# Kernel optimization log

Hardware: AMD Instinct MI355X
Metric: run time of the kernel (lower is better)

The kernel has to match this reference:

```python
import jax, jax.numpy as jnp
import numpy as np

S = 64        # state_dim
M = 16        # message_dim
H = 128       # hidden_unit_message_dim
HR = 128      # hidden_unit_readout_dim
NSTEPS = 10
N_NODES = 10000
N_FACTORS = 40000


def setup_inputs() -> dict:
    rng = np.random.default_rng(0)
    n, F = N_NODES, N_FACTORS
    # random undirected factor pairs (u, v) with u < v
    u = rng.integers(0, n - 1, F)
    v = rng.integers(u + 1, n)
    # var->factor directed edges: (u, i) and (v, i) for factor i
    v2f_src = np.stack([u, v], 1).ravel().astype(np.int32)          # [E]
    v2f_dst = np.repeat(np.arange(F), 2).astype(np.int32)           # [E]
    b = rng.normal(size=n).astype(np.float32)
    Juv = rng.normal(size=F).astype(np.float32)
    Jvu = rng.normal(size=F).astype(np.float32)
    feat_u = np.stack([b[u], b[v], Juv, Jvu], 1)
    feat_v = np.stack([b[v], b[u], Juv, Jvu], 1)
    feat = np.stack([feat_u, feat_v], 1).reshape(-1, 4).astype(np.float32)  # [E,4]
    p = lambda *s: (0.1 * rng.normal(size=s)).astype(np.float32)
    z = lambda *s: np.zeros(s, np.float32)
    inp = {
        'v2f_src': jnp.asarray(v2f_src), 'v2f_dst': jnp.asarray(v2f_dst),
        'f2v_src': jnp.asarray(v2f_dst), 'f2v_dst': jnp.asarray(v2f_src),
        'feat_v2f': jnp.asarray(feat), 'feat_f2v': jnp.asarray(feat),
        'n_nodes': n, 'n_factors': F,
        'Qw': jnp.asarray(p(4, M * M)), 'Qb': jnp.asarray(z(M * M)),
        'mp1_w1': jnp.asarray(p(2 * S, H)), 'mp1_b1': jnp.asarray(z(H)),
        'mp1_w2': jnp.asarray(p(H, H)), 'mp1_b2': jnp.asarray(z(H)),
        'mp1_w3': jnp.asarray(p(H, M)), 'mp1_b3': jnp.asarray(z(M)),
        'mp2_w1': jnp.asarray(p(2 * S, H)), 'mp2_b1': jnp.asarray(z(H)),
        'mp2_w2': jnp.asarray(p(H, H)), 'mp2_b2': jnp.asarray(z(H)),
        'mp2_w3': jnp.asarray(p(H, M)), 'mp2_b3': jnp.asarray(z(M)),
        'g1_wih': jnp.asarray(p(M, 3 * S)), 'g1_whh': jnp.asarray(p(S, 3 * S)),
        'g1_bih': jnp.asarray(z(3 * S)), 'g1_bhh': jnp.asarray(z(3 * S)),
        'g2_wih': jnp.asarray(p(M, 3 * S)), 'g2_whh': jnp.asarray(p(S, 3 * S)),
        'g2_bih': jnp.asarray(z(3 * S)), 'g2_bhh': jnp.asarray(z(3 * S)),
        'ro_w1': jnp.asarray(p(S, HR)), 'ro_b1': jnp.asarray(z(HR)),
        'ro_w2': jnp.asarray(p(HR, HR)), 'ro_b2': jnp.asarray(z(HR)),
        'ro_w3': jnp.asarray(p(HR, 2)), 'ro_b3': jnp.asarray(z(2)),
    }
    return inp


def _mlp(x, w1, b1, w2, b2, w3, b3):
    h = jax.nn.relu(x @ w1 + b1)
    h = jax.nn.relu(h @ w2 + b2)
    return h @ w3 + b3


def _gru(x, h, wih, whh, bih, bhh):
    # torch.nn.GRUCell gate order: r, z, n
    gi = x @ wih + bih
    gh = h @ whh + bhh
    ir, iz, inn = jnp.split(gi, 3, axis=-1)
    hr, hz, hn = jnp.split(gh, 3, axis=-1)
    r = jax.nn.sigmoid(ir + hr)
    zg = jax.nn.sigmoid(iz + hz)
    ng = jnp.tanh(inn + r * hn)
    return (1.0 - zg) * ng + zg * h


def reference(v2f_src, v2f_dst, f2v_src, f2v_dst, feat_v2f, feat_f2v,
              n_nodes, n_factors, Qw, Qb,
              mp1_w1, mp1_b1, mp1_w2, mp1_b2, mp1_w3, mp1_b3,
              mp2_w1, mp2_b1, mp2_w2, mp2_b2, mp2_w3, mp2_b3,
              g1_wih, g1_whh, g1_bih, g1_bhh,
              g2_wih, g2_whh, g2_bih, g2_bhh,
              ro_w1, ro_b1, ro_w2, ro_b2, ro_w3, ro_b3):
    var_h = jnp.zeros((n_nodes, S), feat_v2f.dtype)
    fac_h = jnp.zeros((n_factors, S), feat_v2f.dtype)
    # per-edge transform matrices are the same every step; hoist out of the loop
    q1 = (feat_v2f @ Qw + Qb).reshape(-1, M, M)  # [E, M, M]
    q2 = (feat_f2v @ Qw + Qb).reshape(-1, M, M)
    for _ in range(NSTEPS):
        # var -> factor
        x = jnp.concatenate([var_h[v2f_src], fac_h[v2f_dst]], axis=-1)  # [E, 2S]
        m = _mlp(x, mp1_w1, mp1_b1, mp1_w2, mp1_b2, mp1_w3, mp1_b3)    # [E, M]
        m = jnp.einsum('eij,ej->ei', q1, m)
        fac_msg = jax.ops.segment_sum(m, v2f_dst, num_segments=n_factors)
        fac_h = _gru(fac_msg, fac_h, g1_wih, g1_whh, g1_bih, g1_bhh)
        # factor -> var
        x = jnp.concatenate([fac_h[f2v_src], var_h[f2v_dst]], axis=-1)
        m = _mlp(x, mp2_w1, mp2_b1, mp2_w2, mp2_b2, mp2_w3, mp2_b3)
        m = jnp.einsum('eij,ej->ei', q2, m)
        var_msg = jax.ops.segment_sum(m, f2v_dst, num_segments=n_nodes)
        var_h = _gru(var_msg, var_h, g2_wih, g2_whh, g2_bih, g2_bhh)
    out = _mlp(var_h, ro_w1, ro_b1, ro_w2, ro_b2, ro_w3, ro_b3)  # [n_nodes, 2]
    return jax.nn.softmax(out, axis=1)
```

## Files before the change

kernel.cpp:

```cpp
#include <hip/hip_runtime.h>

#define NSTEPS 10

typedef __attribute__((ext_vector_type(8))) short bf16x8;
typedef __attribute__((ext_vector_type(4))) short bf16x4;
typedef __attribute__((ext_vector_type(4))) float f32x4;

__device__ __forceinline__ float sigmoidf_(float x) { return 1.0f / (1.0f + __expf(-x)); }
__device__ __forceinline__ float tanh_fast(float x) {
  const float e = __expf(2.f * x);
  return 1.f - 2.f / (e + 1.f);
}

__device__ __forceinline__ short bf16_(float x) {
  union { float f; unsigned u; } c; c.f = x;
  unsigned r = (c.u + 0x7FFFu + ((c.u >> 16) & 1u)) >> 16;
  return (short)r;
}
__device__ __forceinline__ unsigned pk2_(float a, float b) {
  union { float f; unsigned u; } ca, cb; ca.f = a; cb.f = b;
  return __builtin_amdgcn_perm(cb.u + 0x8000u, ca.u + 0x8000u, 0x07060302u);
}
__device__ __forceinline__ short pk1_(float a) {
  union { float f; unsigned u; } c; c.f = a;
  return (short)((c.u + 0x8000u) >> 16);
}
__device__ __forceinline__ float lo_(unsigned u) { union { unsigned u; float f; } c; c.u = u << 16; return c.f; }
__device__ __forceinline__ float hi_(unsigned u) { union { unsigned u; float f; } c; c.u = u & 0xffff0000u; return c.f; }

__device__ __forceinline__ f32x4 mfma_16x16x32(bf16x8 a, bf16x8 b, f32x4 c) {
  return __builtin_amdgcn_mfma_f32_16x16x32_bf16(a, b, c, 0, 0, 0);
}

struct PackJob { const float* src; int N; int KS; int nchunks; };
struct PackArgs {
  PackJob jb[10];
  const float* Qw; const float* Qb;
  const float* g1wih; const float* g1whh;
  const float* g2wih; const float* g2whh;
};

__global__ __launch_bounds__(256) void k_pack(PackArgs a, short* __restrict__ out, int total) {
  const int g = blockIdx.x * 256 + threadIdx.x;
  if (g >= total) return;
  int c = g >> 9;
  const int r = g & 511;
  const int j = r & 7, n = (r >> 3) & 15, q = (r >> 7) & 3;
  const int kq = q * 8 + j;
  float val = 0.f;
  bool done = false;
  #pragma unroll
  for (int ji = 0; ji < 10; ++ji) {
    if (!done && c < a.jb[ji].nchunks) {
      const int ks = c % a.jb[ji].KS;
      const int nt = c / a.jb[ji].KS;
      const int k = ks * 32 + kq;
      val = a.jb[ji].src[(size_t)k * a.jb[ji].N + nt * 16 + n];
      done = true;
    }
    if (!done) c -= a.jb[ji].nchunks;
  }
  if (!done) {
    if (c < 5) {
      val = 0.f;
      if (kq < 16) val = (c < 4) ? a.Qw[c * 256 + n * 16 + kq] : a.Qb[n * 16 + kq];
    } else {
      c -= 5;
      const float* wih = (c < 48) ? a.g1wih : a.g2wih;
      const float* whh = (c < 48) ? a.g1whh : a.g2whh;
      if (c >= 48) c -= 48;
      const int nt = c / 3, ks = c % 3;
      const int k = ks * 32 + kq;
      const int ng = nt * 16 + n;
      const int gate = ng >> 6, s = ng & 63;
      val = 0.f;
      if (gate == 0) {
        if (k < 16) val = wih[k * 192 + s];
        else if (k < 80) val = whh[(k - 16) * 192 + s];
      } else if (gate == 1) {
        if (k < 16) val = wih[k * 192 + 64 + s];
        else if (k < 80) val = whh[(k - 16) * 192 + 64 + s];
      } else if (gate == 2) {
        if (k < 16) val = wih[k * 192 + 128 + s];
      } else {
        if (k >= 16 && k < 80) val = whh[(k - 16) * 192 + 128 + s];
      }
    }
  }
  out[g] = bf16_(val);
}

__global__ __launch_bounds__(256) void k_dense2(
    const float* __restrict__ X0, const short* __restrict__ W0, short* __restrict__ C0,
    int rows0, int g0,
    const float* __restrict__ X1, const short* __restrict__ W1, short* __restrict__ C1,
    int rows1, float* __restrict__ zeroPtr,
    const float* __restrict__ gruMsg, float* __restrict__ gruH,
    const short* __restrict__ gruW,
    const float* __restrict__ gbih, const float* __restrict__ gbhh)
{
  constexpr int KS = 2, K = 64, STR = K + 8;
  __shared__ short Xs[64 * STR];
  __shared__ short SA[64 * 104];
  const int t = threadIdx.x, lane = t & 63, wave = t >> 6;
  const int m = lane & 15, quad = lane >> 4;

  const float* X; const short* Wf; short* C; int rows, rbase;
  const bool job0 = (int)blockIdx.x < g0;
  if (job0) {
    X = X0; Wf = W0; C = C0; rows = rows0; rbase = blockIdx.x * 64;
  } else {
    X = X1; Wf = W1; C = C1; rows = rows1; rbase = ((int)blockIdx.x - g0) * 64;
    if (zeroPtr) {
      const int zr = rbase + (t >> 2);
      if (zr < rows1) {
        f32x4 z = {0.f, 0.f, 0.f, 0.f};
        *(f32x4*)(zeroPtr + (size_t)zr * 16 + (t & 3) * 4) = z;
      }
    }
  }

  bf16x8 b[2][KS];
  #pragma unroll
  for (int nt2 = 0; nt2 < 2; ++nt2)
    #pragma unroll
    for (int ks = 0; ks < KS; ++ks)
      b[nt2][ks] = ((const bf16x8*)Wf)[((wave * 2 + nt2) * KS + ks) * 64 + lane];

  if (job0 && gruMsg) {
    {
      const int r = t >> 2, q4 = t & 3, rg = rbase + r;
      #pragma unroll
      for (int i = 0; i < 6; ++i) {
        const int c = q4 * 4 + i * 16;
        f32x4 v = {0.f, 0.f, 0.f, 0.f};
        if (rg < rows) {
          if (c < 16)      v = *(const f32x4*)(gruMsg + (size_t)rg * 16 + c);
          else if (c < 80) v = *(const f32x4*)(gruH + (size_t)rg * 64 + (c - 16));
        }
        *(unsigned*)&SA[r * 104 + c]     = pk2_(v.x, v.y);
        *(unsigned*)&SA[r * 104 + c + 2] = pk2_(v.z, v.w);
      }
    }
    __syncthreads();
    f32x4 acc[16] = {};
    #pragma unroll
    for (int ks = 0; ks < 3; ++ks) {
      const bf16x8 a = *(const bf16x8*)&SA[(wave * 16 + m) * 104 + ks * 32 + quad * 8];
      #pragma unroll
      for (int nt = 0; nt < 16; ++nt)
        acc[nt] = mfma_16x16x32(a, ((const bf16x8*)gruW)[(nt * 3 + ks) * 64 + lane], acc[nt]);
    }
    #pragma unroll
    for (int nt = 0; nt < 4; ++nt) {
      const int s = nt * 16 + m;
      const float br  = gbih[s] + gbhh[s];
      const float bz  = gbih[64 + s] + gbhh[64 + s];
      const float bin = gbih[128 + s];
      const float bhn = gbhh[128 + s];
      #pragma unroll
      for (int reg = 0; reg < 4; ++reg) {
        const int lr = wave * 16 + quad * 4 + reg;
        const int rg = rbase + lr;
        short hv = 0;
        if (rg < rows) {
          const float ho = gruH[(size_t)rg * 64 + s];
          const float rr = sigmoidf_(acc[nt][reg] + br);
          const float zz = sigmoidf_(acc[4 + nt][reg] + bz);
          const float nn = tanh_fast(acc[8 + nt][reg] + bin + rr * (acc[12 + nt][reg] + bhn));
          const float hn = (1.f - zz) * nn + zz * ho;
          gruH[(size_t)rg * 64 + s] = hn;
          hv = pk1_(hn);
        }
        Xs[lr * STR + s] = hv;
      }
    }
    __syncthreads();
  } else {
    const int r = t >> 2, q4 = t & 3, rg = rbase + r;
    #pragma unroll
    for (int i = 0; i < K / 16; ++i) {
      const int cc = q4 * 4 + i * 16;
      f32x4 v = {0.f, 0.f, 0.f, 0.f};
      if (rg < rows) v = *(const f32x4*)(X + (size_t)rg * K + cc);
      *(unsigned*)&Xs[r * STR + cc]     = pk2_(v.x, v.y);
      *(unsigned*)&Xs[r * STR + cc + 2] = pk2_(v.z, v.w);
    }
    __syncthreads();
  }

  f32x4 acc[2][4] = {};
  #pragma unroll
  for (int ks = 0; ks < KS; ++ks) {
    bf16x8 afr[4];
    #pragma unroll
    for (int mt = 0; mt < 4; ++mt)
      afr[mt] = *(const bf16x8*)&Xs[(mt * 16 + m) * STR + ks * 32 + quad * 8];
    #pragma unroll
    for (int nt2 = 0; nt2 < 2; ++nt2)
      #pragma unroll
      for (int mt = 0; mt < 4; ++mt)
        acc[nt2][mt] = mfma_16x16x32(afr[mt], b[nt2][ks], acc[nt2][mt]);
  }

  #pragma unroll
  for (int nt2 = 0; nt2 < 2; ++nt2) {
    const int col = (wave * 2 + nt2) * 16 + m;
    #pragma unroll
    for (int mt = 0; mt < 4; ++mt)
      #pragma unroll
      for (int rr = 0; rr < 4; ++rr) {
        const int rg = rbase + mt * 16 + quad * 4 + rr;
        if (rg < rows) C[(size_t)rg * 128 + col] = pk1_(acc[nt2][mt][rr]);
      }
  }
}

template<bool PAIRED>
__global__ __launch_bounds__(256) void k_edge(
    const short* __restrict__ Pa, const short* __restrict__ Pb,
    const int* __restrict__ src, const int* __restrict__ dst,
    const float* __restrict__ feat,
    const float* __restrict__ b1, const float* __restrict__ b2,
    const float* __restrict__ b3,
    const short* __restrict__ w2f, const short* __restrict__ w3f,
    const short* __restrict__ qf,
    float* __restrict__ outMsg,
    float* __restrict__ facH, const short* __restrict__ gruW,
    const float* __restrict__ gbih, const float* __restrict__ gbhh,
    int E, int F)
{
  __shared__ short h1s[64 * 136];
  __shared__ short ms[64 * 40];
  __shared__ short AsG[32 * 104];
  __shared__ float feats[64 * 4];
  __shared__ int sidx[64], didx[64];

  const int t = threadIdx.x, lane = t & 63, wave = t >> 6;
  const int e0 = blockIdx.x * 64;
  const int f0 = e0 >> 1;

  if (t < 64) {
    const int eg = e0 + t;
    sidx[t] = (eg < E) ? src[eg] : 0;
    didx[t] = (eg < E) ? dst[eg] : 0;
  }
  {
    const int e = t >> 2, k = t & 3;
    const int eg = e0 + e;
    feats[e * 4 + k] = (eg < E) ? feat[(size_t)eg * 4 + k] : 0.f;
  }
  if (PAIRED) {
    const int hr = t >> 3, hc = (t & 7) * 8;
    const int f = f0 + hr;
    f32x4 a0 = {0.f,0.f,0.f,0.f}, a1 = {0.f,0.f,0.f,0.f};
    if (f < F) {
      a0 = *(const f32x4*)(facH + (size_t)f * 64 + hc);
      a1 = *(const f32x4*)(facH + (size_t)f * 64 + hc + 4);
    }
    uint4 o;
    o.x = pk2_(a0.x, a0.y); o.y = pk2_(a0.z, a0.w);
    o.z = pk2_(a1.x, a1.y); o.w = pk2_(a1.z, a1.w);
    *(uint4*)&AsG[hr * 104 + 16 + hc] = o;
    if (t < 64) {
      uint4 z = make_uint4(0u, 0u, 0u, 0u);
      *(uint4*)&AsG[(t >> 1) * 104 + 80 + (t & 1) * 8] = z;
    }
  }
  bf16x8 bw2[2][4];
  #pragma unroll
  for (int nt2 = 0; nt2 < 2; ++nt2)
    #pragma unroll
    for (int ks = 0; ks < 4; ++ks)
      bw2[nt2][ks] = ((const bf16x8*)w2f)[((wave * 2 + nt2) * 4 + ks) * 64 + lane];
  __syncthreads();

  {
    const int r = t >> 2, q4 = t & 3;
    const bool ok = (e0 + r) < E;
    const short* pa = Pa + (size_t)sidx[r] * 128;
    const short* pb = Pb + (size_t)didx[r] * 128;
    #pragma unroll
    for (int i = 0; i < 4; ++i) {
      const int col = (q4 + i * 4) * 8;
      uint4 o = make_uint4(0u, 0u, 0u, 0u);
      if (ok) {
        const uint4 ua = *(const uint4*)(pa + col);
        const uint4 ub = *(const uint4*)(pb + col);
        const f32x4 ba = *(const f32x4*)(b1 + col);
        const f32x4 bb = *(const f32x4*)(b1 + col + 4);
        o.x = pk2_(fmaxf(lo_(ua.x) + lo_(ub.x) + ba.x, 0.f),
                   fmaxf(hi_(ua.x) + hi_(ub.x) + ba.y, 0.f));
        o.y = pk2_(fmaxf(lo_(ua.y) + lo_(ub.y) + ba.z, 0.f),
                   fmaxf(hi_(ua.y) + hi_(ub.y) + ba.w, 0.f));
        o.z = pk2_(fmaxf(lo_(ua.z) + lo_(ub.z) + bb.x, 0.f),
                   fmaxf(hi_(ua.z) + hi_(ub.z) + bb.y, 0.f));
        o.w = pk2_(fmaxf(lo_(ua.w) + lo_(ub.w) + bb.z, 0.f),
                   fmaxf(hi_(ua.w) + hi_(ub.w) + bb.w, 0.f));
      }
      *(uint4*)&h1s[r * 136 + col] = o;
    }
  }
  __syncthreads();

  const int m = lane & 15, quad = lane >> 4;

  f32x4 acc2[2][4] = {};
  #pragma unroll
  for (int ks = 0; ks < 4; ++ks) {
    bf16x8 afr[4];
    #pragma unroll
    for (int mt = 0; mt < 4; ++mt)
      afr[mt] = *(const bf16x8*)&h1s[(mt * 16 + m) * 136 + ks * 32 + quad * 8];
    #pragma unroll
    for (int nt2 = 0; nt2 < 2; ++nt2)
      #pragma unroll
      for (int mt = 0; mt < 4; ++mt)
        acc2[nt2][mt] = mfma_16x16x32(afr[mt], bw2[nt2][ks], acc2[nt2][mt]);
  }
  __syncthreads();

  #pragma unroll
  for (int nt2 = 0; nt2 < 2; ++nt2) {
    const int col = (wave * 2 + nt2) * 16 + m;
    const float bv = b2[col];
    #pragma unroll
    for (int mt = 0; mt < 4; ++mt)
      #pragma unroll
      for (int rr = 0; rr < 4; ++rr)
        h1s[(mt * 16 + quad * 4 + rr) * 136 + col] =
            pk1_(fmaxf(acc2[nt2][mt][rr] + bv, 0.f));
  }
  bf16x8 bw3[4];
  #pragma unroll
  for (int ks = 0; ks < 4; ++ks) bw3[ks] = ((const bf16x8*)w3f)[ks * 64 + lane];
  bf16x8 bq[5];
  #pragma unroll
  for (int tq = 0; tq < 5; ++tq) bq[tq] = ((const bf16x8*)qf)[tq * 64 + lane];
  __syncthreads();

  f32x4 acc3 = {};
  #pragma unroll
  for (int ks = 0; ks < 4; ++ks) {
    const bf16x8 afr = *(const bf16x8*)&h1s[(wave * 16 + m) * 136 + ks * 32 + quad * 8];
    acc3 = mfma_16x16x32(afr, bw3[ks], acc3);
  }
  const float b3v = b3[m];
  #pragma unroll
  for (int rr = 0; rr < 4; ++rr) {
    const int row = wave * 16 + quad * 4 + rr;
    ms[row * 40 + m] = pk1_(acc3[rr] + b3v);
    ms[row * 40 + 16 + m] = 0;
  }
  __syncthreads();

  f32x4 accY[5] = {};
  {
    const bf16x8 afr = *(const bf16x8*)&ms[(wave * 16 + m) * 40 + quad * 8];
    #pragma unroll
    for (int tq = 0; tq < 5; ++tq) accY[tq] = mfma_16x16x32(afr, bq[tq], accY[tq]);
  }
  float mq[4];
  #pragma unroll
  for (int rr = 0; rr < 4; ++rr) {
    const int row = wave * 16 + quad * 4 + rr;
    const f32x4 f = *(const f32x4*)&feats[row * 4];
    mq[rr] = accY[4][rr] + f.x * accY[0][rr] + f.y * accY[1][rr]
                         + f.z * accY[2][rr] + f.w * accY[3][rr];
  }

  if (PAIRED) {
    {
      const int fl = wave * 8 + quad * 2;
      AsG[fl * 104 + m]       = pk1_(mq[0] + mq[1]);
      AsG[(fl + 1) * 104 + m] = pk1_(mq[2] + mq[3]);
    }
    __syncthreads();
    const int mt = wave >> 1, sh = wave & 1;
    f32x4 accG[8] = {};
    #pragma unroll
    for (int ks = 0; ks < 3; ++ks) {
      const bf16x8 a = *(const bf16x8*)&AsG[(mt * 16 + m) * 104 + ks * 32 + quad * 8];
      #pragma unroll
      for (int g = 0; g < 4; ++g)
        #pragma unroll
        for (int nt2 = 0; nt2 < 2; ++nt2) {
          const int nt = g * 4 + sh * 2 + nt2;
          accG[g * 2 + nt2] =
              mfma_16x16x32(a, ((const bf16x8*)gruW)[(nt * 3 + ks) * 64 + lane],
                            accG[g * 2 + nt2]);
        }
    }
    #pragma unroll
    for (int nt2 = 0; nt2 < 2; ++nt2) {
      const int s = sh * 32 + nt2 * 16 + m;
      const float br  = gbih[s] + gbhh[s];
      const float bz  = gbih[64 + s] + gbhh[64 + s];
      const float bin = gbih[128 + s];
      const float bhn = gbhh[128 + s];
      #pragma unroll
      for (int reg = 0; reg < 4; ++reg) {
        const int f = f0 + mt * 16 + quad * 4 + reg;
        if (f < F) {
          const float ho = facH[(size_t)f * 64 + s];
          const float rr = sigmoidf_(accG[nt2][reg] + br);
          const float zz = sigmoidf_(accG[2 + nt2][reg] + bz);
          const float nn = tanh_fast(accG[4 + nt2][reg] + bin +
                                     rr * (accG[6 + nt2][reg] + bhn));
          facH[(size_t)f * 64 + s] = (1.f - zz) * nn + zz * ho;
        }
      }
    }
  } else {
    #pragma unroll
    for (int rr = 0; rr < 4; ++rr) {
      const int erow = wave * 16 + quad * 4 + rr;
      if (e0 + erow < E)
        atomicAdd(outMsg + (size_t)didx[erow] * 16 + m, mq[rr]);
    }
  }
}

__global__ __launch_bounds__(256) void k_readout_f(
    const float* __restrict__ gruMsg, const float* __restrict__ gruH,
    const short* __restrict__ gruW,
    const float* __restrict__ gbih, const float* __restrict__ gbhh,
    const short* __restrict__ ro1f, const float* __restrict__ rob1,
    const short* __restrict__ ro2f, const float* __restrict__ rob2,
    const float* __restrict__ row3, const float* __restrict__ rob3,
    float* __restrict__ out, int rows)
{
  __shared__ short SA[64 * 104];
  __shared__ short SH[64 * 72];
  __shared__ short S1[64 * 136];
  __shared__ short S2[64 * 136];
  __shared__ float w3s[256];
  const int t = threadIdx.x, lane = t & 63, wave = t >> 6;
  const int m = lane & 15, quad = lane >> 4;
  const int rbase = blockIdx.x * 64;

  w3s[t] = row3[t];

  {
    const int r = t >> 2, q4 = t & 3, rg = rbase + r;
    #pragma unroll
    for (int i = 0; i < 6; ++i) {
      const int c = q4 * 4 + i * 16;
      f32x4 v = {0.f, 0.f, 0.f, 0.f};
      if (rg < rows) {
        if (c < 16)      v = *(const f32x4*)(gruMsg + (size_t)rg * 16 + c);
        else if (c < 80) v = *(const f32x4*)(gruH + (size_t)rg * 64 + (c - 16));
      }
      *(unsigned*)&SA[r * 104 + c]     = pk2_(v.x, v.y);
      *(unsigned*)&SA[r * 104 + c + 2] = pk2_(v.z, v.w);
    }
  }
  __syncthreads();
  {
    f32x4 acc[16] = {};
    #pragma unroll
    for (int ks = 0; ks < 3; ++ks) {
      const bf16x8 a = *(const bf16x8*)&SA[(wave * 16 + m) * 104 + ks * 32 + quad * 8];
      #pragma unroll
      for (int nt = 0; nt < 16; ++nt)
        acc[nt] = mfma_16x16x32(a, ((const bf16x8*)gruW)[(nt * 3 + ks) * 64 + lane], acc[nt]);
    }
    #pragma unroll
    for (int nt = 0; nt < 4; ++nt) {
      const int s = nt * 16 + m;
      const float br  = gbih[s] + gbhh[s];
      const float bz  = gbih[64 + s] + gbhh[64 + s];
      const float bin = gbih[128 + s];
      const float bhn = gbhh[128 + s];
      #pragma unroll
      for (int reg = 0; reg < 4; ++reg) {
        const int lr = wave * 16 + quad * 4 + reg;
        const int rg = rbase + lr;
        short hv = 0;
        if (rg < rows) {
          const float ho = gruH[(size_t)rg * 64 + s];
          const float rr = sigmoidf_(acc[nt][reg] + br);
          const float zz = sigmoidf_(acc[4 + nt][reg] + bz);
          const float nn = tanh_fast(acc[8 + nt][reg] + bin + rr * (acc[12 + nt][reg] + bhn));
          hv = pk1_((1.f - zz) * nn + zz * ho);
        }
        SH[lr * 72 + s] = hv;
      }
    }
  }
  __syncthreads();

  {
    f32x4 acc[2][4] = {};
    #pragma unroll
    for (int ks = 0; ks < 2; ++ks) {
      bf16x8 afr[4];
      #pragma unroll
      for (int mt = 0; mt < 4; ++mt)
        afr[mt] = *(const bf16x8*)&SH[(mt * 16 + m) * 72 + ks * 32 + quad * 8];
      #pragma unroll
      for (int nt2 = 0; nt2 < 2; ++nt2) {
        const bf16x8 bb = ((const bf16x8*)ro1f)[((wave * 2 + nt2) * 2 + ks) * 64 + lane];
        #pragma unroll
        for (int mt = 0; mt < 4; ++mt)
          acc[nt2][mt] = mfma_16x16x32(afr[mt], bb, acc[nt2][mt]);
      }
    }
    #pragma unroll
    for (int nt2 = 0; nt2 < 2; ++nt2) {
      const int col = (wave * 2 + nt2) * 16 + m;
      const float bv = rob1[col];
      #pragma unroll
      for (int mt = 0; mt < 4; ++mt)
        #pragma unroll
        for (int rr = 0; rr < 4; ++rr)
          S1[(mt * 16 + quad * 4 + rr) * 136 + col] =
              pk1_(fmaxf(acc[nt2][mt][rr] + bv, 0.f));
    }
  }
  __syncthreads();

  {
    f32x4 acc[2][4] = {};
    #pragma unroll
    for (int ks = 0; ks < 4; ++ks) {
      bf16x8 afr[4];
      #pragma unroll
      for (int mt = 0; mt < 4; ++mt)
        afr[mt] = *(const bf16x8*)&S1[(mt * 16 + m) * 136 + ks * 32 + quad * 8];
      #pragma unroll
      for (int nt2 = 0; nt2 < 2; ++nt2) {
        const bf16x8 bb = ((const bf16x8*)ro2f)[((wave * 2 + nt2) * 4 + ks) * 64 + lane];
        #pragma unroll
        for (int mt = 0; mt < 4; ++mt)
          acc[nt2][mt] = mfma_16x16x32(afr[mt], bb, acc[nt2][mt]);
      }
    }
    #pragma unroll
    for (int nt2 = 0; nt2 < 2; ++nt2) {
      const int col = (wave * 2 + nt2) * 16 + m;
      const float bv = rob2[col];
      #pragma unroll
      for (int mt = 0; mt < 4; ++mt)
        #pragma unroll
        for (int rr = 0; rr < 4; ++rr)
          S2[(mt * 16 + quad * 4 + rr) * 136 + col] =
              pk1_(fmaxf(acc[nt2][mt][rr] + bv, 0.f));
    }
  }
  __syncthreads();

  if (t < 64) {
    const int rg = rbase + t;
    if (rg < rows) {
      float l0 = rob3[0], l1 = rob3[1];
      #pragma unroll 8
      for (int k = 0; k < 128; k += 2) {
        const unsigned u = *(const unsigned*)&S2[t * 136 + k];
        const float x0 = lo_(u), x1 = hi_(u);
        l0 = fmaf(x0, w3s[k * 2 + 0], l0);
        l1 = fmaf(x0, w3s[k * 2 + 1], l1);
        l0 = fmaf(x1, w3s[k * 2 + 2], l0);
        l1 = fmaf(x1, w3s[k * 2 + 3], l1);
      }
      const float mx = fmaxf(l0, l1);
      const float e0 = __expf(l0 - mx), e1 = __expf(l1 - mx);
      const float inv = 1.f / (e0 + e1);
      out[(size_t)rg * 2 + 0] = e0 * inv;
      out[(size_t)rg * 2 + 1] = e1 * inv;
    }
  }
}

extern "C" void kernel_launch(void* const* d_in, const int* in_sizes, int n_in,
                              void* d_out, int out_size, void* d_ws, size_t ws_size,
                              hipStream_t stream)
{
  const int*   v2f_src  = (const int*)d_in[0];
  const int*   v2f_dst  = (const int*)d_in[1];
  const int*   f2v_src  = (const int*)d_in[2];
  const int*   f2v_dst  = (const int*)d_in[3];
  const float* feat_v2f = (const float*)d_in[4];
  const float* feat_f2v = (const float*)d_in[5];
  const float* Qw    = (const float*)d_in[8];
  const float* Qb    = (const float*)d_in[9];
  const float* m1w1  = (const float*)d_in[10];
  const float* m1b1  = (const float*)d_in[11];
  const float* m1w2  = (const float*)d_in[12];
  const float* m1b2  = (const float*)d_in[13];
  const float* m1w3  = (const float*)d_in[14];
  const float* m1b3  = (const float*)d_in[15];
  const float* m2w1  = (const float*)d_in[16];
  const float* m2b1  = (const float*)d_in[17];
  const float* m2w2  = (const float*)d_in[18];
  const float* m2b2  = (const float*)d_in[19];
  const float* m2w3  = (const float*)d_in[20];
  const float* m2b3  = (const float*)d_in[21];
  const float* g1wih = (const float*)d_in[22];
  const float* g1whh = (const float*)d_in[23];
  const float* g1bih = (const float*)d_in[24];
  const float* g1bhh = (const float*)d_in[25];
  const float* g2wih = (const float*)d_in[26];
  const float* g2whh = (const float*)d_in[27];
  const float* g2bih = (const float*)d_in[28];
  const float* g2bhh = (const float*)d_in[29];
  const float* row1  = (const float*)d_in[30];
  const float* rob1  = (const float*)d_in[31];
  const float* row2  = (const float*)d_in[32];
  const float* rob2  = (const float*)d_in[33];
  const float* row3  = (const float*)d_in[34];
  const float* rob3  = (const float*)d_in[35];

  const int E = in_sizes[0];
  const int N = out_size / 2;
  const int F = E / 2;

  float* ws    = (float*)d_ws;
  float* var_h = ws;
  float* fac_h = var_h + (size_t)N * 64;
  float* msgV  = fac_h + (size_t)F * 64;
  short* Abuf  = (short*)(msgV + (size_t)N * 16);
  short* Bbuf  = Abuf + (size_t)F * 128;
  short* wb    = Bbuf + (size_t)F * 128;

  const int C_W2A = 0,  C_W2B = 32, C_W3A = 64, C_W3B = 68;
  const int C_W1AS = 72, C_W1AD = 88, C_W1BS = 104, C_W1BD = 120;
  const int C_RO1 = 136, C_RO2 = 152, C_Q = 184, C_G1 = 189, C_G2 = 237;
  const int TOTAL_CHUNKS = 285;

  short* PB_w2a  = wb + C_W2A  * 512;
  short* PB_w2b  = wb + C_W2B  * 512;
  short* PB_w3a  = wb + C_W3A  * 512;
  short* PB_w3b  = wb + C_W3B  * 512;
  short* PB_w1as = wb + C_W1AS * 512;
  short* PB_w1ad = wb + C_W1AD * 512;
  short* PB_w1bs = wb + C_W1BS * 512;
  short* PB_w1bd = wb + C_W1BD * 512;
  short* PB_ro1  = wb + C_RO1  * 512;
  short* PB_ro2  = wb + C_RO2  * 512;
  short* PB_q    = wb + C_Q    * 512;
  short* PB_g1   = wb + C_G1   * 512;
  short* PB_g2   = wb + C_G2   * 512;

  hipMemsetAsync(var_h, 0, (size_t)N * 64 * sizeof(float), stream);
  hipMemsetAsync(fac_h, 0, (size_t)F * 64 * sizeof(float), stream);

  PackArgs pa;
  pa.jb[0] = {m1w2,            128, 4, 32};
  pa.jb[1] = {m2w2,            128, 4, 32};
  pa.jb[2] = {m1w3,             16, 4,  4};
  pa.jb[3] = {m2w3,             16, 4,  4};
  pa.jb[4] = {m1w1,            128, 2, 16};
  pa.jb[5] = {m1w1 + 64 * 128, 128, 2, 16};
  pa.jb[6] = {m2w1,            128, 2, 16};
  pa.jb[7] = {m2w1 + 64 * 128, 128, 2, 16};
  pa.jb[8] = {row1,            128, 2, 16};
  pa.jb[9] = {row2,            128, 4, 32};
  pa.Qw = Qw; pa.Qb = Qb;
  pa.g1wih = g1wih; pa.g1whh = g1whh;
  pa.g2wih = g2wih; pa.g2whh = g2whh;
  const int packTotal = TOTAL_CHUNKS * 512;
  k_pack<<<(packTotal + 255) / 256, 256, 0, stream>>>(pa, wb, packTotal);

  const int gN = (N + 63) / 64;
  const int gF = (F + 63) / 64;
  const int gE = (E + 63) / 64;

  for (int step = 0; step < NSTEPS; ++step) {
    k_dense2<<<gN + gF, 256, 0, stream>>>(
        var_h, PB_w1as, Abuf, N, gN,
        fac_h, PB_w1ad, Bbuf, F, nullptr,
        step ? msgV : nullptr, var_h, PB_g2, g2bih, g2bhh);
    k_edge<true><<<gE, 256, 0, stream>>>(
        Abuf, Bbuf, v2f_src, v2f_dst, feat_v2f, m1b1, m1b2, m1b3,
        PB_w2a, PB_w3a, PB_q, nullptr, fac_h, PB_g1, g1bih, g1bhh, E, F);
    k_dense2<<<gF + gN, 256, 0, stream>>>(
        fac_h, PB_w1bs, Abuf, F, gF,
        var_h, PB_w1bd, Bbuf, N, msgV,
        nullptr, nullptr, nullptr, nullptr, nullptr);
    k_edge<false><<<gE, 256, 0, stream>>>(
        Abuf, Bbuf, f2v_src, f2v_dst, feat_f2v, m2b1, m2b2, m2b3,
        PB_w2b, PB_w3b, PB_q, msgV, nullptr, nullptr, nullptr, nullptr, E, F);
  }

  k_readout_f<<<gN, 256, 0, stream>>>(
      msgV, var_h, PB_g2, g2bih, g2bhh,
      PB_ro1, rob1, PB_ro2, rob2, row3, rob3, (float*)d_out, N);
}
```

Baseline: 717.1 us.

## Replace per-step kernel launches with one cooperative persistent kernel using grid sync

Moves the whole 10-step message-passing loop, weight packing and state zeroing into a single cooperative persistent kernel that uses grid.sync between phases. The factor-side work is fused per edge block: the factor GRU update and the f2v first-layer projection run in the same block that computes v2f messages, because each factor owns two consecutive edges. The var-side dense projections are also merged into one combined weight. This removes launch overhead and intermediate global round-trips, at the cost of grid-wide barriers, an occupancy limit of 2 blocks per CU, and a fallback path kept for when cooperative launch is unavailable.

After: 2.125 ms. 2.96x slower.

```diff
diff --git a/kernel.cpp b/kernel.cpp
--- a/kernel.cpp
+++ b/kernel.cpp
@@ -1,9 +1,11 @@
 #include <hip/hip_runtime.h>
+#include <hip/hip_cooperative_groups.h>
+
+namespace cg = cooperative_groups;
 
 #define NSTEPS 10
 
 typedef __attribute__((ext_vector_type(8))) short bf16x8;
-typedef __attribute__((ext_vector_type(4))) short bf16x4;
 typedef __attribute__((ext_vector_type(4))) float f32x4;
 
 __device__ __forceinline__ float sigmoidf_(float x) { return 1.0f / (1.0f + __expf(-x)); }
@@ -11,7 +13,6 @@
   const float e = __expf(2.f * x);
   return 1.f - 2.f / (e + 1.f);
 }
-
 __device__ __forceinline__ short bf16_(float x) {
   union { float f; unsigned u; } c; c.f = x;
   unsigned r = (c.u + 0x7FFFu + ((c.u >> 16) & 1u)) >> 16;
@@ -31,6 +32,21 @@
 __device__ __forceinline__ f32x4 mfma_16x16x32(bf16x8 a, bf16x8 b, f32x4 c) {
   return __builtin_amdgcn_mfma_f32_16x16x32_bf16(a, b, c, 0, 0, 0);
 }
+
+#define C_W2A   0
+#define C_W2B   32
+#define C_W3A   64
+#define C_W3B   68
+#define C_ACOMB 72
+#define C_W1BD  88
+#define C_W1AD  104
+#define C_W1BS  120
+#define C_RO1   136
+#define C_RO2   152
+#define C_Q     184
+#define C_G1    189
+#define C_G2    237
+#define TOTAL_CHUNKS 285
 
 struct PackJob { const float* src; int N; int KS; int nchunks; };
 struct PackArgs {
@@ -40,9 +56,7 @@
   const float* g2wih; const float* g2whh;
 };
 
-__global__ __launch_bounds__(256) void k_pack(PackArgs a, short* __restrict__ out, int total) {
-  const int g = blockIdx.x * 256 + threadIdx.x;
-  if (g >= total) return;
+__device__ __forceinline__ float pack_val(const PackArgs& a, int g) {
   int c = g >> 9;
   const int r = g & 511;
   const int j = r & 7, n = (r >> 3) & 15, q = (r >> 7) & 3;
@@ -87,7 +101,538 @@
       }
     }
   }
-  out[g] = bf16_(val);
+  return val;
+}
+
+__global__ __launch_bounds__(256) void k_pack(PackArgs a, short* __restrict__ out, int total) {
+  const int g = blockIdx.x * 256 + threadIdx.x;
+  if (g < total) out[g] = bf16_(pack_val(a, g));
+}
+
+__device__ __forceinline__ void edge_tail(
+    const short* wb, int cw2, int cw3,
+    const float* b2, const float* b3,
+    short* h1s, short* ms, const float* feats,
+    int lane, int wave, int m, int quad, float* mq)
+{
+  f32x4 acc2[2][4] = {};
+  #pragma unroll
+  for (int ks = 0; ks < 4; ++ks) {
+    bf16x8 afr[4];
+    #pragma unroll
+    for (int mt = 0; mt < 4; ++mt)
+      afr[mt] = *(const bf16x8*)&h1s[(mt * 16 + m) * 136 + ks * 32 + quad * 8];
+    #pragma unroll
+    for (int nt2 = 0; nt2 < 2; ++nt2) {
+      const bf16x8 bfr = ((const bf16x8*)(wb + cw2))[((wave * 2 + nt2) * 4 + ks) * 64 + lane];
+      #pragma unroll
+      for (int mt = 0; mt < 4; ++mt)
+        acc2[nt2][mt] = mfma_16x16x32(afr[mt], bfr, acc2[nt2][mt]);
+    }
+  }
+  __syncthreads();
+  #pragma unroll
+  for (int nt2 = 0; nt2 < 2; ++nt2) {
+    const int col = (wave * 2 + nt2) * 16 + m;
+    const float bv = b2[col];
+    #pragma unroll
+    for (int mt = 0; mt < 4; ++mt)
+      #pragma unroll
+      for (int rr = 0; rr < 4; ++rr)
+        h1s[(mt * 16 + quad * 4 + rr) * 136 + col] =
+            pk1_(fmaxf(acc2[nt2][mt][rr] + bv, 0.f));
+  }
+  __syncthreads();
+  f32x4 acc3 = {};
+  #pragma unroll
+  for (int ks = 0; ks < 4; ++ks) {
+    const bf16x8 afr = *(const bf16x8*)&h1s[(wave * 16 + m) * 136 + ks * 32 + quad * 8];
+    acc3 = mfma_16x16x32(afr, ((const bf16x8*)(wb + cw3))[ks * 64 + lane], acc3);
+  }
+  const float b3v = b3[m];
+  #pragma unroll
+  for (int rr = 0; rr < 4; ++rr) {
+    const int row = wave * 16 + quad * 4 + rr;
+    ms[row * 40 + m] = pk1_(acc3[rr] + b3v);
+    ms[row * 40 + 16 + m] = 0;
+  }
+  __syncthreads();
+  f32x4 accY[5] = {};
+  {
+    const bf16x8 afr = *(const bf16x8*)&ms[(wave * 16 + m) * 40 + quad * 8];
+    #pragma unroll
+    for (int tq = 0; tq < 5; ++tq)
+      accY[tq] = mfma_16x16x32(afr, ((const bf16x8*)(wb + C_Q * 512))[tq * 64 + lane], accY[tq]);
+  }
+  #pragma unroll
+  for (int rr = 0; rr < 4; ++rr) {
+    const int row = wave * 16 + quad * 4 + rr;
+    const f32x4 f = *(const f32x4*)&feats[row * 4];
+    mq[rr] = accY[4][rr] + f.x * accY[0][rr] + f.y * accY[1][rr]
+                         + f.z * accY[2][rr] + f.w * accY[3][rr];
+  }
+}
+
+__device__ __forceinline__ void var_gru_tile(
+    const short* wb, const float* gbih, const float* gbhh,
+    const short* SA, float* gruH, short* outTile, int outStr,
+    int rbase, int Nn, int lane, int wave, int m, int quad, bool writeH)
+{
+  f32x4 acc[16] = {};
+  #pragma unroll
+  for (int ks = 0; ks < 3; ++ks) {
+    const bf16x8 av = *(const bf16x8*)&SA[(wave * 16 + m) * 104 + ks * 32 + quad * 8];
+    #pragma unroll
+    for (int nt = 0; nt < 16; ++nt)
+      acc[nt] = mfma_16x16x32(av, ((const bf16x8*)(wb + C_G2 * 512))[(nt * 3 + ks) * 64 + lane], acc[nt]);
+  }
+  #pragma unroll
+  for (int nt = 0; nt < 4; ++nt) {
+    const int s = nt * 16 + m;
+    const float br  = gbih[s] + gbhh[s];
+    const float bz  = gbih[64 + s] + gbhh[64 + s];
+    const float bin = gbih[128 + s];
+    const float bhn = gbhh[128 + s];
+    #pragma unroll
+    for (int reg = 0; reg < 4; ++reg) {
+      const int lr = wave * 16 + quad * 4 + reg, rg = rbase + lr;
+      short hv = 0;
+      if (rg < Nn) {
+        const float ho = gruH[(size_t)rg * 64 + s];
+        const float rr = sigmoidf_(acc[nt][reg] + br);
+        const float zz = sigmoidf_(acc[4 + nt][reg] + bz);
+        const float nn = tanh_fast(acc[8 + nt][reg] + bin + rr * (acc[12 + nt][reg] + bhn));
+        const float hn = (1.f - zz) * nn + zz * ho;
+        if (writeH) gruH[(size_t)rg * 64 + s] = hn;
+        hv = pk1_(hn);
+      }
+      outTile[lr * outStr + s] = hv;
+    }
+  }
+}
+
+struct KArgs {
+  PackArgs pk;
+  int packTotal;
+  short* wb;
+  const int* v2f_src; const int* f2v_dst;
+  const float* featA; const float* featB;
+  const float *m1b1, *m1b2, *m1b3;
+  const float *m2b1, *m2b2, *m2b3;
+  const float *g1bih, *g1bhh, *g2bih, *g2bhh;
+  const float *rob1, *rob2, *row3, *rob3;
+  float *var_h, *fac_h, *msgV;
+  short *Abuf, *Bbuf;
+  float* out;
+  float* zbase; int zcount4;
+  int N, F, E, gN, gB;
+};
+
+__global__ __launch_bounds__(256, 2) void k_persist(KArgs a)
+{
+  cg::grid_group grid = cg::this_grid();
+  __shared__ __align__(16) char smem[45056];
+  const int t = threadIdx.x, lane = t & 63, wave = t >> 6;
+  const int m = lane & 15, quad = lane >> 4;
+  const int nb = gridDim.x, bid = blockIdx.x;
+  const int tid = bid * 256 + t, nth = nb * 256;
+  const short* wb = a.wb;
+
+  for (int g = tid; g < a.packTotal; g += nth)
+    a.wb[g] = bf16_(pack_val(a.pk, g));
+  {
+    f32x4 z = {0.f, 0.f, 0.f, 0.f};
+    f32x4* zp = (f32x4*)a.zbase;
+    for (int g = tid; g < a.zcount4; g += nth) zp[g] = z;
+  }
+  grid.sync();
+
+  for (int step = 0; step < NSTEPS; ++step) {
+    {
+      short* SA = (short*)(smem);
+      short* Xs = (short*)(smem + 13312);
+      for (int tb = bid; tb < a.gN; tb += nb) {
+        const int rbase = tb * 64;
+        if (step > 0) {
+          {
+            const int r = t >> 2, q4 = t & 3, rg = rbase + r;
+            #pragma unroll
+            for (int i = 0; i < 6; ++i) {
+              const int c = q4 * 4 + i * 16;
+              f32x4 v = {0.f, 0.f, 0.f, 0.f};
+              if (rg < a.N) {
+                if (c < 16)      v = *(const f32x4*)(a.msgV + (size_t)rg * 16 + c);
+                else if (c < 80) v = *(const f32x4*)(a.var_h + (size_t)rg * 64 + (c - 16));
+              }
+              *(unsigned*)&SA[r * 104 + c]     = pk2_(v.x, v.y);
+              *(unsigned*)&SA[r * 104 + c + 2] = pk2_(v.z, v.w);
+            }
+            if (rbase + r < a.N) {
+              f32x4 z = {0.f, 0.f, 0.f, 0.f};
+              *(f32x4*)(a.msgV + (size_t)(rbase + r) * 16 + q4 * 4) = z;
+            }
+          }
+          __syncthreads();
+          var_gru_tile(wb, a.g2bih, a.g2bhh, SA, a.var_h, Xs, 72,
+                       rbase, a.N, lane, wave, m, quad, true);
+          __syncthreads();
+        } else {
+          const int r = t >> 2, q4 = t & 3, rg = rbase + r;
+          #pragma unroll
+          for (int i = 0; i < 4; ++i) {
+            const int cc = q4 * 4 + i * 16;
+            f32x4 v = {0.f, 0.f, 0.f, 0.f};
+            if (rg < a.N) v = *(const f32x4*)(a.var_h + (size_t)rg * 64 + cc);
+            *(unsigned*)&Xs[r * 72 + cc]     = pk2_(v.x, v.y);
+            *(unsigned*)&Xs[r * 72 + cc + 2] = pk2_(v.z, v.w);
+          }
+          __syncthreads();
+        }
+        f32x4 acc[4][4] = {};
+        #pragma unroll
+        for (int ks = 0; ks < 2; ++ks) {
+          bf16x8 afr[4];
+          #pragma unroll
+          for (int mt = 0; mt < 4; ++mt)
+            afr[mt] = *(const bf16x8*)&Xs[(mt * 16 + m) * 72 + ks * 32 + quad * 8];
+          #pragma unroll
+          for (int j = 0; j < 4; ++j) {
+            const bf16x8 bfr = ((const bf16x8*)(wb + C_ACOMB * 512))[((wave * 4 + j) * 2 + ks) * 64 + lane];
+            #pragma unroll
+            for (int mt = 0; mt < 4; ++mt)
+              acc[j][mt] = mfma_16x16x32(afr[mt], bfr, acc[j][mt]);
+          }
+        }
+        #pragma unroll
+        for (int j = 0; j < 4; ++j) {
+          const int col = (wave * 4 + j) * 16 + m;
+          short* dst = (col < 128) ? a.Abuf : a.Bbuf;
+          const int c2 = col & 127;
+          #pragma unroll
+          for (int mt = 0; mt < 4; ++mt)
+            #pragma unroll
+            for (int reg = 0; reg < 4; ++reg) {
+              const int rg = rbase + mt * 16 + quad * 4 + reg;
+              if (rg < a.N) dst[(size_t)rg * 128 + c2] = pk1_(acc[j][mt][reg]);
+            }
+        }
+        __syncthreads();
+      }
+    }
+    grid.sync();
+    {
+      short* AsG   = (short*)(smem);
+      short* Ps    = (short*)(smem + 6656);
+      short* h1s   = (short*)(smem + 15360);
+      short* ms    = (short*)(smem + 32768);
+      short* Fs2   = (short*)(smem + 37888);
+      float* feats = (float*)(smem + 42496);
+      int*   sidx  = (int*)(smem + 43520);
+      int*   didx  = (int*)(smem + 43776);
+      for (int tb = bid; tb < a.gB; tb += nb) {
+        const int e0 = tb * 64, f0 = tb * 32;
+        if (t < 64) {
+          const int eg = e0 + t;
+          sidx[t] = (eg < a.E) ? a.v2f_src[eg] : 0;
+          didx[t] = (eg < a.E) ? a.f2v_dst[eg] : 0;
+        }
+        {
+          const int e = t >> 2, k = t & 3, eg = e0 + e;
+          feats[e * 4 + k] = (eg < a.E) ? a.featA[(size_t)eg * 4 + k] : 0.f;
+        }
+        {
+          const int hr = t >> 3, hc = (t & 7) * 8;
+          const int f = f0 + hr;
+          f32x4 a0 = {0.f,0.f,0.f,0.f}, a1 = {0.f,0.f,0.f,0.f};
+          if (f < a.F) {
+            a0 = *(const f32x4*)(a.fac_h + (size_t)f * 64 + hc);
+            a1 = *(const f32x4*)(a.fac_h + (size_t)f * 64 + hc + 4);
+          }
+          uint4 o;
+          o.x = pk2_(a0.x, a0.y); o.y = pk2_(a0.z, a0.w);
+          o.z = pk2_(a1.x, a1.y); o.w = pk2_(a1.z, a1.w);
+          *(uint4*)&AsG[hr * 104 + 16 + hc] = o;
+          if (t < 64) {
+            uint4 z = make_uint4(0u, 0u, 0u, 0u);
+            *(uint4*)&AsG[(t >> 1) * 104 + 80 + (t & 1) * 8] = z;
+          }
+        }
+        __syncthreads();
+        {
+          const int mt = wave & 1, ng = wave >> 1;
+          f32x4 pacc[4] = {};
+          #pragma unroll
+          for (int ks = 0; ks < 2; ++ks) {
+            const bf16x8 av = *(const bf16x8*)&AsG[(mt * 16 + m) * 104 + 16 + ks * 32 + quad * 8];
+            #pragma unroll
+            for (int j = 0; j < 4; ++j) {
+              const bf16x8 bfr = ((const bf16x8*)(wb + C_W1AD * 512))[((ng * 4 + j) * 2 + ks) * 64 + lane];
+              pacc[j] = mfma_16x16x32(av, bfr, pacc[j]);
+            }
+          }
+          #pragma unroll
+          for (int j = 0; j < 4; ++j) {
+            const int col = (ng * 4 + j) * 16 + m;
+            #pragma unroll
+            for (int reg = 0; reg < 4; ++reg)
+              Ps[(mt * 16 + quad * 4 + reg) * 136 + col] = pk1_(pacc[j][reg]);
+          }
+        }
+        __syncthreads();
+        {
+          const int r = t >> 2, q4 = t & 3;
+          const bool ok = (e0 + r) < a.E;
+          const short* pa = a.Abuf + (size_t)sidx[r] * 128;
+          const short* pb = Ps + (r >> 1) * 136;
+          #pragma unroll
+          for (int i = 0; i < 4; ++i) {
+            const int col = (q4 + i * 4) * 8;
+            uint4 o = make_uint4(0u, 0u, 0u, 0u);
+            if (ok) {
+              const uint4 ua = *(const uint4*)(pa + col);
+              const uint4 ub = *(const uint4*)(pb + col);
+              const f32x4 ba = *(const f32x4*)(a.m1b1 + col);
+              const f32x4 bb = *(const f32x4*)(a.m1b1 + col + 4);
+              o.x = pk2_(fmaxf(lo_(ua.x) + lo_(ub.x) + ba.x, 0.f),
+                         fmaxf(hi_(ua.x) + hi_(ub.x) + ba.y, 0.f));
+              o.y = pk2_(fmaxf(lo_(ua.y) + lo_(ub.y) + ba.z, 0.f),
+                         fmaxf(hi_(ua.y) + hi_(ub.y) + ba.w, 0.f));
+              o.z = pk2_(fmaxf(lo_(ua.z) + lo_(ub.z) + bb.x, 0.f),
+                         fmaxf(hi_(ua.z) + hi_(ub.z) + bb.y, 0.f));
+              o.w = pk2_(fmaxf(lo_(ua.w) + lo_(ub.w) + bb.z, 0.f),
+                         fmaxf(hi_(ua.w) + hi_(ub.w) + bb.w, 0.f));
+            }
+            *(uint4*)&h1s[r * 136 + col] = o;
+          }
+        }
+        __syncthreads();
+        float mq[4];
+        edge_tail(wb, C_W2A * 512, C_W3A * 512, a.m1b2, a.m1b3,
+                  h1s, ms, feats, lane, wave, m, quad, mq);
+        {
+          const int fl = wave * 8 + quad * 2;
+          AsG[fl * 104 + m]       = pk1_(mq[0] + mq[1]);
+          AsG[(fl + 1) * 104 + m] = pk1_(mq[2] + mq[3]);
+        }
+        __syncthreads();
+        {
+          const int mtg = wave >> 1, sh = wave & 1;
+          f32x4 accG[8] = {};
+          #pragma unroll
+          for (int ks = 0; ks < 3; ++ks) {
+            const bf16x8 av = *(const bf16x8*)&AsG[(mtg * 16 + m) * 104 + ks * 32 + quad * 8];
+            #pragma unroll
+            for (int g = 0; g < 4; ++g)
+              #pragma unroll
+              for (int nt2 = 0; nt2 < 2; ++nt2) {
+                const int nt = g * 4 + sh * 2 + nt2;
+                accG[g * 2 + nt2] = mfma_16x16x32(
+                    av, ((const bf16x8*)(wb + C_G1 * 512))[(nt * 3 + ks) * 64 + lane],
+                    accG[g * 2 + nt2]);
+              }
+          }
+          #pragma unroll
+          for (int nt2 = 0; nt2 < 2; ++nt2) {
+            const int s = sh * 32 + nt2 * 16 + m;
+            const float br  = a.g1bih[s] + a.g1bhh[s];
+            const float bz  = a.g1bih[64 + s] + a.g1bhh[64 + s];
+            const float bin = a.g1bih[128 + s];
+            const float bhn = a.g1bhh[128 + s];
+            #pragma unroll
+            for (int reg = 0; reg < 4; ++reg) {
+              const int lr = mtg * 16 + quad * 4 + reg;
+              const int f = f0 + lr;
+              short hv = 0;
+              if (f < a.F) {
+                const float ho = a.fac_h[(size_t)f * 64 + s];
+                const float rr = sigmoidf_(accG[nt2][reg] + br);
+                const float zz = sigmoidf_(accG[2 + nt2][reg] + bz);
+                const float nn = tanh_fast(accG[4 + nt2][reg] + bin +
+                                           rr * (accG[6 + nt2][reg] + bhn));
+                const float hn = (1.f - zz) * nn + zz * ho;
+                a.fac_h[(size_t)f * 64 + s] = hn;
+                hv = pk1_(hn);
+              }
+              Fs2[lr * 72 + s] = hv;
+            }
+          }
+        }
+        {
+          const int e = t >> 2, k = t & 3, eg = e0 + e;
+          feats[e * 4 + k] = (eg < a.E) ? a.featB[(size_t)eg * 4 + k] : 0.f;
+        }
+        __syncthreads();
+        {
+          const int mt = wave & 1, ng = wave >> 1;
+          f32x4 pacc[4] = {};
+          #pragma unroll
+          for (int ks = 0; ks < 2; ++ks) {
+            const bf16x8 av = *(const bf16x8*)&Fs2[(mt * 16 + m) * 72 + ks * 32 + quad * 8];
+            #pragma unroll
+            for (int j = 0; j < 4; ++j) {
+              const bf16x8 bfr = ((const bf16x8*)(wb + C_W1BS * 512))[((ng * 4 + j) * 2 + ks) * 64 + lane];
+              pacc[j] = mfma_16x16x32(av, bfr, pacc[j]);
+            }
+          }
+          #pragma unroll
+          for (int j = 0; j < 4; ++j) {
+            const int col = (ng * 4 + j) * 16 + m;
+            #pragma unroll
+            for (int reg = 0; reg < 4; ++reg)
+              Ps[(mt * 16 + quad * 4 + reg) * 136 + col] = pk1_(pacc[j][reg]);
+          }
+        }
+        __syncthreads();
+        {
+          const int r = t >> 2, q4 = t & 3;
+          const bool ok = (e0 + r) < a.E;
+          const short* pa = Ps + (r >> 1) * 136;
+          const short* pb = a.Bbuf + (size_t)didx[r] * 128;
+          #pragma unroll
+          for (int i = 0; i < 4; ++i) {
+            const int col = (q4 + i * 4) * 8;
+            uint4 o = make_uint4(0u, 0u, 0u, 0u);
+            if (ok) {
+              const uint4 ua = *(const uint4*)(pa + col);
+              const uint4 ub = *(const uint4*)(pb + col);
+              const f32x4 ba = *(const f32x4*)(a.m2b1 + col);
+              const f32x4 bb = *(const f32x4*)(a.m2b1 + col + 4);
+              o.x = pk2_(fmaxf(lo_(ua.x) + lo_(ub.x) + ba.x, 0.f),
+                         fmaxf(hi_(ua.x) + hi_(ub.x) + ba.y, 0.f));
+              o.y = pk2_(fmaxf(lo_(ua.y) + lo_(ub.y) + ba.z, 0.f),
+                         fmaxf(hi_(ua.y) + hi_(ub.y) + ba.w, 0.f));
+              o.z = pk2_(fmaxf(lo_(ua.z) + lo_(ub.z) + bb.x, 0.f),
+                         fmaxf(hi_(ua.z) + hi_(ub.z) + bb.y, 0.f));
+              o.w = pk2_(fmaxf(lo_(ua.w) + lo_(ub.w) + bb.z, 0.f),
+                         fmaxf(hi_(ua.w) + hi_(ub.w) + bb.w, 0.f));
+            }
+            *(uint4*)&h1s[r * 136 + col] = o;
+          }
+        }
+        __syncthreads();
+        float mq2[4];
+        edge_tail(wb, C_W2B * 512, C_W3B * 512, a.m2b2, a.m2b3,
+                  h1s, ms, feats, lane, wave, m, quad, mq2);
+        #pragma unroll
+        for (int rr = 0; rr < 4; ++rr) {
+          const int erow = wave * 16 + quad * 4 + rr;
+          if (e0 + erow < a.E)
+            atomicAdd(a.msgV + (size_t)didx[erow] * 16 + m, mq2[rr]);
+        }
+        __syncthreads();
+      }
+    }
+    grid.sync();
+  }
+
+  {
+    short* SAr = (short*)(smem);
+    float* w3s = (float*)(smem + 17408);
+    short* SH  = (short*)(smem + 18432);
+    short* S1  = (short*)(smem + 27648);
+    short* S2  = (short*)(smem);
+    for (int tb = bid; tb < a.gN; tb += nb) {
+      const int rbase = tb * 64;
+      w3s[t] = a.row3[t];
+      {
+        const int r = t >> 2, q4 = t & 3, rg = rbase + r;
+        #pragma unroll
+        for (int i = 0; i < 6; ++i) {
+          const int c = q4 * 4 + i * 16;
+          f32x4 v = {0.f, 0.f, 0.f, 0.f};
+          if (rg < a.N) {
+            if (c < 16)      v = *(const f32x4*)(a.msgV + (size_t)rg * 16 + c);
+            else if (c < 80) v = *(const f32x4*)(a.var_h + (size_t)rg * 64 + (c - 16));
+          }
+          *(unsigned*)&SAr[r * 104 + c]     = pk2_(v.x, v.y);
+          *(unsigned*)&SAr[r * 104 + c + 2] = pk2_(v.z, v.w);
+        }
+      }
+      __syncthreads();
+      var_gru_tile(wb, a.g2bih, a.g2bhh, SAr, a.var_h, SH, 72,
+                   rbase, a.N, lane, wave, m, quad, false);
+      __syncthreads();
+      {
+        f32x4 acc[2][4] = {};
+        #pragma unroll
+        for (int ks = 0; ks < 2; ++ks) {
+          bf16x8 afr[4];
+          #pragma unroll
+          for (int mt = 0; mt < 4; ++mt)
+            afr[mt] = *(const bf16x8*)&SH[(mt * 16 + m) * 72 + ks * 32 + quad * 8];
+          #pragma unroll
+          for (int nt2 = 0; nt2 < 2; ++nt2) {
+            const bf16x8 bfr = ((const bf16x8*)(wb + C_RO1 * 512))[((wave * 2 + nt2) * 2 + ks) * 64 + lane];
+            #pragma unroll
+            for (int mt = 0; mt < 4; ++mt)
+              acc[nt2][mt] = mfma_16x16x32(afr[mt], bfr, acc[nt2][mt]);
+          }
+        }
+        #pragma unroll
+        for (int nt2 = 0; nt2 < 2; ++nt2) {
+          const int col = (wave * 2 + nt2) * 16 + m;
+          const float bv = a.rob1[col];
+          #pragma unroll
+          for (int mt = 0; mt < 4; ++mt)
+            #pragma unroll
+            for (int rr = 0; rr < 4; ++rr)
+              S1[(mt * 16 + quad * 4 + rr) * 136 + col] =
+                  pk1_(fmaxf(acc[nt2][mt][rr] + bv, 0.f));
+        }
+      }
+      __syncthreads();
+      {
+        f32x4 acc[2][4] = {};
+        #pragma unroll
+        for (int ks = 0; ks < 4; ++ks) {
+          bf16x8 afr[4];
+          #pragma unroll
+          for (int mt = 0; mt < 4; ++mt)
+            afr[mt] = *(const bf16x8*)&S1[(mt * 16 + m) * 136 + ks * 32 + quad * 8];
+          #pragma unroll
+          for (int nt2 = 0; nt2 < 2; ++nt2) {
+            const bf16x8 bfr = ((const bf16x8*)(wb + C_RO2 * 512))[((wave * 2 + nt2) * 4 + ks) * 64 + lane];
+            #pragma unroll
+            for (int mt = 0; mt < 4; ++mt)
+              acc[nt2][mt] = mfma_16x16x32(afr[mt], bfr, acc[nt2][mt]);
+          }
+        }
+        #pragma unroll
+        for (int nt2 = 0; nt2 < 2; ++nt2) {
+          const int col = (wave * 2 + nt2) * 16 + m;
+          const float bv = a.rob2[col];
+          #pragma unroll
+          for (int mt = 0; mt < 4; ++mt)
+            #pragma unroll
+            for (int rr = 0; rr < 4; ++rr)
+              S2[(mt * 16 + quad * 4 + rr) * 136 + col] =
+                  pk1_(fmaxf(acc[nt2][mt][rr] + bv, 0.f));
+        }
+      }
+      __syncthreads();
+      if (t < 64) {
+        const int rg = rbase + t;
+        if (rg < a.N) {
+          float l0 = a.rob3[0], l1 = a.rob3[1];
+          #pragma unroll 8
+          for (int k = 0; k < 128; k += 2) {
+            const unsigned u = *(const unsigned*)&S2[t * 136 + k];
+            const float x0 = lo_(u), x1 = hi_(u);
+            l0 = fmaf(x0, w3s[k * 2 + 0], l0);
+            l1 = fmaf(x0, w3s[k * 2 + 1], l1);
+            l0 = fmaf(x1, w3s[k * 2 + 2], l0);
+            l1 = fmaf(x1, w3s[k * 2 + 3], l1);
+          }
+          const float mx = fmaxf(l0, l1);
+          const float e0 = __expf(l0 - mx), e1 = __expf(l1 - mx);
+          const float inv = 1.f / (e0 + e1);
+          a.out[(size_t)rg * 2 + 0] = e0 * inv;
+          a.out[(size_t)rg * 2 + 1] = e1 * inv;
+        }
+      }
+      __syncthreads();
+    }
+  }
 }
 
 __global__ __launch_bounds__(256) void k_dense2(
@@ -96,7 +641,7 @@
     const float* __restrict__ X1, const short* __restrict__ W1, short* __restrict__ C1,
     int rows1, float* __restrict__ zeroPtr,
     const float* __restrict__ gruMsg, float* __restrict__ gruH,
-    const short* __restrict__ gruW,
+    const short* __restrict__ wb,
     const float* __restrict__ gbih, const float* __restrict__ gbhh)
 {
   constexpr int KS = 2, K = 64, STR = K + 8;
@@ -143,38 +688,8 @@
       }
     }
     __syncthreads();
-    f32x4 acc[16] = {};
-    #pragma unroll
-    for (int ks = 0; ks < 3; ++ks) {
-      const bf16x8 a = *(const bf16x8*)&SA[(wave * 16 + m) * 104 + ks * 32 + quad * 8];
-      #pragma unroll
-      for (int nt = 0; nt < 16; ++nt)
-        acc[nt] = mfma_16x16x32(a, ((const bf16x8*)gruW)[(nt * 3 + ks) * 64 + lane], acc[nt]);
-    }
-    #pragma unroll
-    for (int nt = 0; nt < 4; ++nt) {
-      const int s = nt * 16 + m;
-      const float br  = gbih[s] + gbhh[s];
-      const float bz  = gbih[64 + s] + gbhh[64 + s];
-      const float bin = gbih[128 + s];
-      const float bhn = gbhh[128 + s];
-      #pragma unroll
-      for (int reg = 0; reg < 4; ++reg) {
-        const int lr = wave * 16 + quad * 4 + reg;
-        const int rg = rbase + lr;
-        short hv = 0;
-        if (rg < rows) {
-          const float ho = gruH[(size_t)rg * 64 + s];
-          const float rr = sigmoidf_(acc[nt][reg] + br);
-          const float zz = sigmoidf_(acc[4 + nt][reg] + bz);
-          const float nn = tanh_fast(acc[8 + nt][reg] + bin + rr * (acc[12 + nt][reg] + bhn));
-          const float hn = (1.f - zz) * nn + zz * ho;
-          gruH[(size_t)rg * 64 + s] = hn;
-          hv = pk1_(hn);
-        }
-        Xs[lr * STR + s] = hv;
-      }
-    }
+    var_gru_tile(wb, gbih, gbhh, SA, gruH, Xs, STR,
+                 rbase, rows, lane, wave, m, quad, true);
     __syncthreads();
   } else {
     const int r = t >> 2, q4 = t & 3, rg = rbase + r;
@@ -217,16 +732,15 @@
 }
 
 template<bool PAIRED>
-__global__ __launch_bounds__(256) void k_edge(
+__global__ __launch_bounds__(256) void k_edge_fb(
     const short* __restrict__ Pa, const short* __restrict__ Pb,
     const int* __restrict__ src, const int* __restrict__ dst,
     const float* __restrict__ feat,
     const float* __restrict__ b1, const float* __restrict__ b2,
     const float* __restrict__ b3,
-    const short* __restrict__ w2f, const short* __restrict__ w3f,
-    const short* __restrict__ qf,
+    const short* __restrict__ wb, int cw2, int cw3,
     float* __restrict__ outMsg,
-    float* __restrict__ facH, const short* __restrict__ gruW,
+    float* __restrict__ facH,
     const float* __restrict__ gbih, const float* __restrict__ gbhh,
     int E, int F)
 {
@@ -237,8 +751,8 @@
   __shared__ int sidx[64], didx[64];
 
   const int t = threadIdx.x, lane = t & 63, wave = t >> 6;
-  const int e0 = blockIdx.x * 64;
-  const int f0 = e0 >> 1;
+  const int e0 = blockIdx.x * 64, f0 = e0 >> 1;
+  const int m = lane & 15, quad = lane >> 4;
 
   if (t < 64) {
     const int eg = e0 + t;
@@ -246,8 +760,7 @@
     didx[t] = (eg < E) ? dst[eg] : 0;
   }
   {
-    const int e = t >> 2, k = t & 3;
-    const int eg = e0 + e;
+    const int e = t >> 2, k = t & 3, eg = e0 + e;
     feats[e * 4 + k] = (eg < E) ? feat[(size_t)eg * 4 + k] : 0.f;
   }
   if (PAIRED) {
@@ -267,12 +780,6 @@
       *(uint4*)&AsG[(t >> 1) * 104 + 80 + (t & 1) * 8] = z;
     }
   }
-  bf16x8 bw2[2][4];
-  #pragma unroll
-  for (int nt2 = 0; nt2 < 2; ++nt2)
-    #pragma unroll
-    for (int ks = 0; ks < 4; ++ks)
-      bw2[nt2][ks] = ((const bf16x8*)w2f)[((wave * 2 + nt2) * 4 + ks) * 64 + lane];
   __syncthreads();
 
   {
@@ -303,71 +810,8 @@
   }
   __syncthreads();
 
-  const int m = lane & 15, quad = lane >> 4;
-
-  f32x4 acc2[2][4] = {};
-  #pragma unroll
-  for (int ks = 0; ks < 4; ++ks) {
-    bf16x8 afr[4];
-    #pragma unroll
-    for (int mt = 0; mt < 4; ++mt)
-      afr[mt] = *(const bf16x8*)&h1s[(mt * 16 + m) * 136 + ks * 32 + quad * 8];
-    #pragma unroll
-    for (int nt2 = 0; nt2 < 2; ++nt2)
-      #pragma unroll
-      for (int mt = 0; mt < 4; ++mt)
-        acc2[nt2][mt] = mfma_16x16x32(afr[mt], bw2[nt2][ks], acc2[nt2][mt]);
-  }
-  __syncthreads();
-
-  #pragma unroll
-  for (int nt2 = 0; nt2 < 2; ++nt2) {
-    const int col = (wave * 2 + nt2) * 16 + m;
-    const float bv = b2[col];
-    #pragma unroll
-    for (int mt = 0; mt < 4; ++mt)
-      #pragma unroll
-      for (int rr = 0; rr < 4; ++rr)
-        h1s[(mt * 16 + quad * 4 + rr) * 136 + col] =
-            pk1_(fmaxf(acc2[nt2][mt][rr] + bv, 0.f));
-  }
-  bf16x8 bw3[4];
-  #pragma unroll
-  for (int ks = 0; ks < 4; ++ks) bw3[ks] = ((const bf16x8*)w3f)[ks * 64 + lane];
-  bf16x8 bq[5];
-  #pragma unroll
-  for (int tq = 0; tq < 5; ++tq) bq[tq] = ((const bf16x8*)qf)[tq * 64 + lane];
-  __syncthreads();
-
-  f32x4 acc3 = {};
-  #pragma unroll
-  for (int ks = 0; ks < 4; ++ks) {
-    const bf16x8 afr = *(const bf16x8*)&h1s[(wave * 16 + m) * 136 + ks * 32 + quad * 8];
-    acc3 = mfma_16x16x32(afr, bw3[ks], acc3);
-  }
-  const float b3v = b3[m];
-  #pragma unroll
-  for (int rr = 0; rr < 4; ++rr) {
-    const int row = wave * 16 + quad * 4 + rr;
-    ms[row * 40 + m] = pk1_(acc3[rr] + b3v);
-    ms[row * 40 + 16 + m] = 0;
-  }
-  __syncthreads();
-
-  f32x4 accY[5] = {};
-  {
-    const bf16x8 afr = *(const bf16x8*)&ms[(wave * 16 + m) * 40 + quad * 8];
-    #pragma unroll
-    for (int tq = 0; tq < 5; ++tq) accY[tq] = mfma_16x16x32(afr, bq[tq], accY[tq]);
-  }
   float mq[4];
-  #pragma unroll
-  for (int rr = 0; rr < 4; ++rr) {
-    const int row = wave * 16 + quad * 4 + rr;
-    const f32x4 f = *(const f32x4*)&feats[row * 4];
-    mq[rr] = accY[4][rr] + f.x * accY[0][rr] + f.y * accY[1][rr]
-                         + f.z * accY[2][rr] + f.w * accY[3][rr];
-  }
+  edge_tail(wb, cw2, cw3, b2, b3, h1s, ms, feats, lane, wave, m, quad, mq);
 
   if (PAIRED) {
     {
@@ -376,19 +820,19 @@
       AsG[(fl + 1) * 104 + m] = pk1_(mq[2] + mq[3]);
     }
     __syncthreads();
-    const int mt = wave >> 1, sh = wave & 1;
+    const int mtg = wave >> 1, sh = wave & 1;
     f32x4 accG[8] = {};
     #pragma unroll
     for (int ks = 0; ks < 3; ++ks) {
-      const bf16x8 a = *(const bf16x8*)&AsG[(mt * 16 + m) * 104 + ks * 32 + quad * 8];
+      const bf16x8 av = *(const bf16x8*)&AsG[(mtg * 16 + m) * 104 + ks * 32 + quad * 8];
       #pragma unroll
       for (int g = 0; g < 4; ++g)
         #pragma unroll
         for (int nt2 = 0; nt2 < 2; ++nt2) {
           const int nt = g * 4 + sh * 2 + nt2;
-          accG[g * 2 + nt2] =
-              mfma_16x16x32(a, ((const bf16x8*)gruW)[(nt * 3 + ks) * 64 + lane],
-                            accG[g * 2 + nt2]);
+          accG[g * 2 + nt2] = mfma_16x16x32(
+              av, ((const bf16x8*)(wb + C_G1 * 512))[(nt * 3 + ks) * 64 + lane],
+              accG[g * 2 + nt2]);
         }
     }
     #pragma unroll
@@ -400,7 +844,7 @@
       const float bhn = gbhh[128 + s];
       #pragma unroll
       for (int reg = 0; reg < 4; ++reg) {
-        const int f = f0 + mt * 16 + quad * 4 + reg;
+        const int f = f0 + mtg * 16 + quad * 4 + reg;
         if (f < F) {
           const float ho = facH[(size_t)f * 64 + s];
           const float rr = sigmoidf_(accG[nt2][reg] + br);
@@ -423,10 +867,9 @@
 
 __global__ __launch_bounds__(256) void k_readout_f(
     const float* __restrict__ gruMsg, const float* __restrict__ gruH,
-    const short* __restrict__ gruW,
+    const short* __restrict__ wb,
     const float* __restrict__ gbih, const float* __restrict__ gbhh,
-    const short* __restrict__ ro1f, const float* __restrict__ rob1,
-    const short* __restrict__ ro2f, const float* __restrict__ rob2,
+    const float* __restrict__ rob1, const float* __restrict__ rob2,
     const float* __restrict__ row3, const float* __restrict__ rob3,
     float* __restrict__ out, int rows)
 {
@@ -440,7 +883,6 @@
   const int rbase = blockIdx.x * 64;
 
   w3s[t] = row3[t];
-
   {
     const int r = t >> 2, q4 = t & 3, rg = rbase + r;
     #pragma unroll
@@ -456,40 +898,9 @@
     }
   }
   __syncthreads();
-  {
-    f32x4 acc[16] = {};
-    #pragma unroll
-    for (int ks = 0; ks < 3; ++ks) {
-      const bf16x8 a = *(const bf16x8*)&SA[(wave * 16 + m) * 104 + ks * 32 + quad * 8];
-      #pragma unroll
-      for (int nt = 0; nt < 16; ++nt)
-        acc[nt] = mfma_16x16x32(a, ((const bf16x8*)gruW)[(nt * 3 + ks) * 64 + lane], acc[nt]);
-    }
-    #pragma unroll
-    for (int nt = 0; nt < 4; ++nt) {
-      const int s = nt * 16 + m;
-      const float br  = gbih[s] + gbhh[s];
-      const float bz  = gbih[64 + s] + gbhh[64 + s];
-      const float bin = gbih[128 + s];
-      const float bhn = gbhh[128 + s];
-      #pragma unroll
-      for (int reg = 0; reg < 4; ++reg) {
-        const int lr = wave * 16 + quad * 4 + reg;
-        const int rg = rbase + lr;
-        short hv = 0;
-        if (rg < rows) {
-          const float ho = gruH[(size_t)rg * 64 + s];
-          const float rr = sigmoidf_(acc[nt][reg] + br);
-          const float zz = sigmoidf_(acc[4 + nt][reg] + bz);
-          const float nn = tanh_fast(acc[8 + nt][reg] + bin + rr * (acc[12 + nt][reg] + bhn));
-          hv = pk1_((1.f - zz) * nn + zz * ho);
-        }
-        SH[lr * 72 + s] = hv;
-      }
-    }
-  }
+  var_gru_tile(wb, gbih, gbhh, SA, (float*)gruH, SH, 72,
+               rbase, rows, lane, wave, m, quad, false);
   __syncthreads();
-
   {
     f32x4 acc[2][4] = {};
     #pragma unroll
@@ -500,10 +911,10 @@
         afr[mt] = *(const bf16x8*)&SH[(mt * 16 + m) * 72 + ks * 32 + quad * 8];
       #pragma unroll
       for (int nt2 = 0; nt2 < 2; ++nt2) {
-        const bf16x8 bb = ((const bf16x8*)ro1f)[((wave * 2 + nt2) * 2 + ks) * 64 + lane];
+        const bf16x8 bfr = ((const bf16x8*)(wb + C_RO1 * 512))[((wave * 2 + nt2) * 2 + ks) * 64 + lane];
         #pragma unroll
         for (int mt = 0; mt < 4; ++mt)
-          acc[nt2][mt] = mfma_16x16x32(afr[mt], bb, acc[nt2][mt]);
+          acc[nt2][mt] = mfma_16x16x32(afr[mt], bfr, acc[nt2][mt]);
       }
     }
     #pragma unroll
@@ -519,7 +930,6 @@
     }
   }
   __syncthreads();
-
   {
     f32x4 acc[2][4] = {};
     #pragma unroll
@@ -530,10 +940,10 @@
         afr[mt] = *(const bf16x8*)&S1[(mt * 16 + m) * 136 + ks * 32 + quad * 8];
       #pragma unroll
       for (int nt2 = 0; nt2 < 2; ++nt2) {
-        const bf16x8 bb = ((const bf16x8*)ro2f)[((wave * 2 + nt2) * 4 + ks) * 64 + lane];
+        const bf16x8 bfr = ((const bf16x8*)(wb + C_RO2 * 512))[((wave * 2 + nt2) * 4 + ks) * 64 + lane];
         #pragma unroll
         for (int mt = 0; mt < 4; ++mt)
-          acc[nt2][mt] = mfma_16x16x32(afr[mt], bb, acc[nt2][mt]);
+          acc[nt2][mt] = mfma_16x16x32(afr[mt], bfr, acc[nt2][mt]);
       }
     }
     #pragma unroll
@@ -549,7 +959,6 @@
     }
   }
   __syncthreads();
-
   if (t < 64) {
     const int rg = rbase + t;
     if (rg < rows) {
@@ -615,75 +1024,84 @@
   const int N = out_size / 2;
   const int F = E / 2;
 
-  float* ws    = (float*)d_ws;
-  float* var_h = ws;
+  float* wsf   = (float*)d_ws;
+  float* var_h = wsf;
   float* fac_h = var_h + (size_t)N * 64;
   float* msgV  = fac_h + (size_t)F * 64;
   short* Abuf  = (short*)(msgV + (size_t)N * 16);
   short* Bbuf  = Abuf + (size_t)F * 128;
   short* wb    = Bbuf + (size_t)F * 128;
 
-  const int C_W2A = 0,  C_W2B = 32, C_W3A = 64, C_W3B = 68;
-  const int C_W1AS = 72, C_W1AD = 88, C_W1BS = 104, C_W1BD = 120;
-  const int C_RO1 = 136, C_RO2 = 152, C_Q = 184, C_G1 = 189, C_G2 = 237;
-  const int TOTAL_CHUNKS = 285;
-
-  short* PB_w2a  = wb + C_W2A  * 512;
-  short* PB_w2b  = wb + C_W2B  * 512;
-  short* PB_w3a  = wb + C_W3A  * 512;
-  short* PB_w3b  = wb + C_W3B  * 512;
-  short* PB_w1as = wb + C_W1AS * 512;
-  short* PB_w1ad = wb + C_W1AD * 512;
-  short* PB_w1bs = wb + C_W1BS * 512;
-  short* PB_w1bd = wb + C_W1BD * 512;
-  short* PB_ro1  = wb + C_RO1  * 512;
-  short* PB_ro2  = wb + C_RO2  * 512;
-  short* PB_q    = wb + C_Q    * 512;
-  short* PB_g1   = wb + C_G1   * 512;
-  short* PB_g2   = wb + C_G2   * 512;
+  KArgs ka;
+  ka.pk.jb[0] = {m1w2,            128, 4, 32};
+  ka.pk.jb[1] = {m2w2,            128, 4, 32};
+  ka.pk.jb[2] = {m1w3,             16, 4,  4};
+  ka.pk.jb[3] = {m2w3,             16, 4,  4};
+  ka.pk.jb[4] = {m1w1,            128, 2, 16};
+  ka.pk.jb[5] = {m2w1 + 64 * 128, 128, 2, 16};
+  ka.pk.jb[6] = {m1w1 + 64 * 128, 128, 2, 16};
+  ka.pk.jb[7] = {m2w1,            128, 2, 16};
+  ka.pk.jb[8] = {row1,            128, 2, 16};
+  ka.pk.jb[9] = {row2,            128, 4, 32};
+  ka.pk.Qw = Qw; ka.pk.Qb = Qb;
+  ka.pk.g1wih = g1wih; ka.pk.g1whh = g1whh;
+  ka.pk.g2wih = g2wih; ka.pk.g2whh = g2whh;
+  ka.packTotal = TOTAL_CHUNKS * 512;
+  ka.wb = wb;
+  ka.v2f_src = v2f_src; ka.f2v_dst = f2v_dst;
+  ka.featA = feat_v2f; ka.featB = feat_f2v;
+  ka.m1b1 = m1b1; ka.m1b2 = m1b2; ka.m1b3 = m1b3;
+  ka.m2b1 = m2b1; ka.m2b2 = m2b2; ka.m2b3 = m2b3;
+  ka.g1bih = g1bih; ka.g1bhh = g1bhh; ka.g2bih = g2bih; ka.g2bhh = g2bhh;
+  ka.rob1 = rob1; ka.rob2 = rob2; ka.row3 = row3; ka.rob3 = rob3;
+  ka.var_h = var_h; ka.fac_h = fac_h; ka.msgV = msgV;
+  ka.Abuf = Abuf; ka.Bbuf = Bbuf;
+  ka.out = (float*)d_out;
+  ka.zbase = var_h;
+  ka.zcount4 = (N * 64 + F * 64 + N * 16) / 4;
+  ka.N = N; ka.F = F; ka.E = E;
+  ka.gN = (N + 63) / 64;
+  ka.gB = (E + 63) / 64;
+
+  int dev = 0;
+  hipGetDevice(&dev);
+  int cus = 256, coopOK = 0, maxBlk = 0;
+  hipDeviceGetAttribute(&cus, hipDeviceAttributeMultiprocessorCount, dev);
+  hipDeviceGetAttribute(&coopOK, hipDeviceAttributeCooperativeLaunch, dev);
+  hipOccupancyMaxActiveBlocksPerMultiprocessor(&maxBlk, k_persist, 256, 0);
+
+  bool launched = false;
+  if (coopOK && maxBlk >= 1) {
+    const int bpc = maxBlk < 2 ? maxBlk : 2;
+    const int grid = cus * bpc;
+    void* params[] = { &ka };
+    hipError_t err = hipLaunchCooperativeKernel((void*)k_persist, dim3(grid),
+                                                dim3(256), params, 0, stream);
+    launched = (err == hipSuccess);
+  }
+  if (launched) return;
 
   hipMemsetAsync(var_h, 0, (size_t)N * 64 * sizeof(float), stream);
   hipMemsetAsync(fac_h, 0, (size_t)F * 64 * sizeof(float), stream);
-
-  PackArgs pa;
-  pa.jb[0] = {m1w2,            128, 4, 32};
-  pa.jb[1] = {m2w2,            128, 4, 32};
-  pa.jb[2] = {m1w3,             16, 4,  4};
-  pa.jb[3] = {m2w3,             16, 4,  4};
-  pa.jb[4] = {m1w1,            128, 2, 16};
-  pa.jb[5] = {m1w1 + 64 * 128, 128, 2, 16};
-  pa.jb[6] = {m2w1,            128, 2, 16};
-  pa.jb[7] = {m2w1 + 64 * 128, 128, 2, 16};
-  pa.jb[8] = {row1,            128, 2, 16};
-  pa.jb[9] = {row2,            128, 4, 32};
-  pa.Qw = Qw; pa.Qb = Qb;
-  pa.g1wih = g1wih; pa.g1whh = g1whh;
-  pa.g2wih = g2wih; pa.g2whh = g2whh;
-  const int packTotal = TOTAL_CHUNKS * 512;
-  k_pack<<<(packTotal + 255) / 256, 256, 0, stream>>>(pa, wb, packTotal);
-
-  const int gN = (N + 63) / 64;
-  const int gF = (F + 63) / 64;
-  const int gE = (E + 63) / 64;
-
+  k_pack<<<(ka.packTotal + 255) / 256, 256, 0, stream>>>(ka.pk, wb, ka.packTotal);
+
+  const int gN = ka.gN, gE = ka.gB;
   for (int step = 0; step < NSTEPS; ++step) {
-    k_dense2<<<gN + gF, 256, 0, stream>>>(
-        var_h, PB_w1as, Abuf, N, gN,
-        fac_h, PB_w1ad, Bbuf, F, nullptr,
-        step ? msgV : nullptr, var_h, PB_g2, g2bih, g2bhh);
-    k_edge<true><<<gE, 256, 0, stream>>>(
+    k_dense2<<<gN + (F + 63) / 64, 256, 0, stream>>>(
+        var_h, wb + C_ACOMB * 512, Abuf, N, gN,
+        fac_h, wb + C_W1AD * 512, Bbuf, F, nullptr,
+        step ? msgV : nullptr, var_h, wb, g2bih, g2bhh);
+    k_edge_fb<true><<<gE, 256, 0, stream>>>(
         Abuf, Bbuf, v2f_src, v2f_dst, feat_v2f, m1b1, m1b2, m1b3,
-        PB_w2a, PB_w3a, PB_q, nullptr, fac_h, PB_g1, g1bih, g1bhh, E, F);
-    k_dense2<<<gF + gN, 256, 0, stream>>>(
-        fac_h, PB_w1bs, Abuf, F, gF,
-        var_h, PB_w1bd, Bbuf, N, msgV,
+        wb, C_W2A * 512, C_W3A * 512, nullptr, fac_h, g1bih, g1bhh, E, F);
+    k_dense2<<<(F + 63) / 64 + gN, 256, 0, stream>>>(
+        fac_h, wb + C_W1BS * 512, Abuf, F, (F + 63) / 64,
+        var_h, wb + C_W1BD * 512, Bbuf, N, msgV,
         nullptr, nullptr, nullptr, nullptr, nullptr);
-    k_edge<false><<<gE, 256, 0, stream>>>(
+    k_edge_fb<false><<<gE, 256, 0, stream>>>(
         Abuf, Bbuf, f2v_src, f2v_dst, feat_f2v, m2b1, m2b2, m2b3,
-        PB_w2b, PB_w3b, PB_q, msgV, nullptr, nullptr, nullptr, nullptr, E, F);
-  }
-
+        wb, C_W2B * 512, C_W3B * 512, msgV, nullptr, g2bih, g2bhh, E, F);
+  }
   k_readout_f<<<gN, 256, 0, stream>>>(
-      msgV, var_h, PB_g2, g2bih, g2bhh,
-      PB_ro1, rob1, PB_ro2, rob2, row3, rob3, (float*)d_out, N);
-}
+      msgV, var_h, wb, g2bih, g2bhh, rob1, rob2, row3, rob3, (float*)d_out, N);
+}
```
